# Kernel tuning notes

Hardware: AMD Instinct MI355X
Metric: run time of the kernel (lower is better)

## Reference

```python
import jax, jax.numpy as jnp
import numpy as np

NU, MI, D, H, DH, L, LAYERS = 80000, 40000, 64, 8, 8, 2, 3
EUI, EII, DT, DI, B = 1600000, 400000, 768, 512, 512


def setup_inputs() -> dict:
    rng = np.random.default_rng(0)
    u = rng.integers(0, NU, EUI); it = rng.integers(0, MI, EUI)
    du = np.maximum(np.bincount(u, minlength=NU), 1)
    di = np.maximum(np.bincount(it, minlength=MI), 1)
    val = (1.0 / np.sqrt(du[u] * di[it])).astype(np.float32)
    g_row = np.concatenate([u, it + NU]).astype(np.int32)
    g_col = np.concatenate([it + NU, u]).astype(np.int32)
    g_val = np.concatenate([val, val])

    def ig(seed):  # random item-item graph + self loops (dgl.add_self_loop)
        r = np.random.default_rng(seed)
        s = r.integers(0, MI, EII); d = r.integers(0, MI, EII); sl = np.arange(MI)
        return np.concatenate([s, sl]).astype(np.int32), np.concatenate([d, sl]).astype(np.int32)
    t_src, t_dst = ig(1); i_src, i_dst = ig(2)

    def xav(*shape):
        lim = np.sqrt(6.0 / (shape[-2] + shape[-1]))
        return rng.uniform(-lim, lim, shape).astype(np.float32)

    inp = dict(
        user_emb=(rng.standard_normal((NU, D)) * 0.1).astype(np.float32),
        item_emb=(rng.standard_normal((MI, D)) * 0.1).astype(np.float32),
        g_row=g_row, g_col=g_col, g_val=g_val,
        txt_feat=rng.standard_normal((MI, DT)).astype(np.float32),
        img_feat=rng.standard_normal((MI, DI)).astype(np.float32),
        t_src=t_src, t_dst=t_dst, i_src=i_src, i_dst=i_dst,
        txt_proj_w=xav(DT, D), txt_proj_b=np.zeros(D, np.float32),
        txt_fc_w=xav(L, D, D), txt_attn_l=xav(L, H, DH), txt_attn_r=xav(L, H, DH),
        txt_bias=np.zeros((L, D), np.float32),
        img_proj_w=xav(DI, D), img_proj_b=np.zeros(D, np.float32),
        img_fc_w=xav(L, D, D), img_attn_l=xav(L, H, DH), img_attn_r=xav(L, H, DH),
        img_bias=np.zeros((L, D), np.float32),
        delta_img=xav(D, D), delta_txt=xav(D, D),
        alpha=np.float32(0.05), beta=np.float32(0.8),
        ln_g=np.ones(D, np.float32), ln_b=np.zeros(D, np.float32),
        users=rng.integers(0, NU, B).astype(np.int32),
    )
    return {k: jnp.asarray(v) for k, v in inp.items()}


def _spmm(row, col, val, x, n):
    return jax.ops.segment_sum(val[:, None] * x[col], row, num_segments=n)


def _gat_layer(x, src, dst, fc_w, al, ar, b):
    N = x.shape[0]
    h = (x @ fc_w).reshape(N, H, DH)                 # [N,H,Dh]
    el = jnp.einsum('nhd,hd->nh', h, al)
    er = jnp.einsum('nhd,hd->nh', h, ar)
    e = jax.nn.leaky_relu(el[src] + er[dst], 0.2)    # [E,H]
    m = jax.ops.segment_max(e, dst, num_segments=N)
    a = jnp.exp(e - m[dst])
    a = a / jax.ops.segment_sum(a, dst, num_segments=N)[dst]
    out = jax.ops.segment_sum(a[:, :, None] * h[src], dst, num_segments=N)
    return (out + b.reshape(1, H, DH)).reshape(N, H * DH)


def _branch(feat, src, dst, pw, pb, fcw, al, ar, bias):
    x = feat @ pw + pb
    for l in range(L):
        x = jax.nn.leaky_relu(_gat_layer(x, src, dst, fcw[l], al[l], ar[l], bias[l]), 0.2)
    return x


def _sinkhorn(C, eps=0.01, iters=100):
    K = jnp.exp(-C / eps)
    d1, d2 = C.shape
    mu = jnp.full((d1,), 1.0 / d1, C.dtype)
    nu = jnp.full((d2,), 1.0 / d2, C.dtype)
    def body(_, uv):
        u, v = uv
        u = mu / (K @ v + 1e-8)
        v = nu / (K.T @ u + 1e-8)
        return (u, v)
    u, v = jax.lax.fori_loop(0, iters, body, (mu, nu))
    return u[:, None] * K * v[None, :]


def _ot_align(mm, st, delta):
    I = mm.shape[0]
    # mean_i (mm[i,k]-st[i,l])^2 * scale, without materializing [I,D,D]
    C = ((mm * mm).mean(0)[:, None] + (st * st).mean(0)[None, :] - 2.0 * (mm.T @ st) / I) * 100.0
    T = jax.lax.stop_gradient(_sinkhorn(C))  # torch computes T under no_grad
    return mm @ (T + delta)


def reference(user_emb, item_emb, g_row, g_col, g_val, txt_feat, img_feat,
              t_src, t_dst, i_src, i_dst,
              txt_proj_w, txt_proj_b, txt_fc_w, txt_attn_l, txt_attn_r, txt_bias,
              img_proj_w, img_proj_b, img_fc_w, img_attn_l, img_attn_r, img_bias,
              delta_img, delta_txt, alpha, beta, ln_g, ln_b, users):
    # LightGCN propagation
    cur = jnp.concatenate([user_emb, item_emb], 0)
    acc = cur
    for _ in range(LAYERS):
        cur = _spmm(g_row, g_col, g_val, cur, NU + MI)
        acc = acc + cur
    light = acc / (LAYERS + 1)
    zu, zi_cf = light[:NU], light[NU:]
    # multimodal GAT branches (dropout = eval mode)
    zi_txt = _branch(txt_feat, t_src, t_dst, txt_proj_w, txt_proj_b, txt_fc_w, txt_attn_l, txt_attn_r, txt_bias)
    zi_img = _branch(img_feat, i_src, i_dst, img_proj_w, img_proj_b, img_fc_w, img_attn_l, img_attn_r, img_bias)
    # OAT fusion
    a_img = _ot_align(zi_img, zi_cf, delta_img)
    a_txt = _ot_align(zi_txt, zi_cf, delta_txt)
    z = (1.0 - alpha - beta) * zi_cf + alpha * a_img + beta * a_txt
    mu = z.mean(-1, keepdims=True)
    var = ((z - mu) ** 2).mean(-1, keepdims=True)
    z = (z - mu) / jnp.sqrt(var + 1e-5) * ln_g + ln_b
    z = z / jnp.maximum(jnp.linalg.norm(z, axis=-1, keepdims=True), 1e-12)
    return zu[users] @ z.T  # [B, M_items] ratings
```

## Files before the change

### kernel.cpp

```cpp
#include <hip/hip_runtime.h>
#include <math.h>

__device__ __forceinline__ float lrelu(float x) { return x >= 0.f ? x : 0.2f * x; }

__global__ void hist_k(const int* __restrict__ row, int* __restrict__ tick, int E) {
  int e = blockIdx.x * 256 + threadIdx.x;
  if (e >= E) return;
  atomicAdd(&tick[row[e]], 1);
}

__global__ __launch_bounds__(256) void scan_part_k(const int* __restrict__ tick,
                                                   int* __restrict__ part, int N) {
  __shared__ int red[256];
  int base = blockIdx.x * 4096;
  int s = 0;
  for (int i = threadIdx.x; i < 4096; i += 256) {
    int idx = base + i;
    if (idx < N) s += tick[idx];
  }
  red[threadIdx.x] = s;
  __syncthreads();
  for (int off = 128; off > 0; off >>= 1) {
    if (threadIdx.x < off) red[threadIdx.x] += red[threadIdx.x + off];
    __syncthreads();
  }
  if (threadIdx.x == 0) part[blockIdx.x] = red[0];
}

__global__ __launch_bounds__(1024) void scan_partials_k(int* __restrict__ part, int nb) {
  __shared__ int sh[1024];
  int t = threadIdx.x;
  int v = (t < nb) ? part[t] : 0;
  sh[t] = v;
  __syncthreads();
  for (int off = 1; off < 1024; off <<= 1) {
    int x = sh[t];
    int y = (t >= off) ? sh[t - off] : 0;
    __syncthreads();
    sh[t] = x + y;
    __syncthreads();
  }
  if (t < nb) part[t] = (t == 0) ? 0 : sh[t - 1];
  if (t == 0) part[nb] = sh[nb - 1];
}

__global__ __launch_bounds__(256) void scan_apply_k(int* __restrict__ tick, int* __restrict__ rs,
                                                    const int* __restrict__ part, int N, int nb) {
  __shared__ int th[256];
  int base = blockIdx.x * 4096;
  int lo = base + threadIdx.x * 16;
  int vals[16];
  int s = 0;
#pragma unroll
  for (int j = 0; j < 16; ++j) {
    int idx = lo + j;
    int v = (idx < N) ? tick[idx] : 0;
    vals[j] = v;
    s += v;
  }
  th[threadIdx.x] = s;
  __syncthreads();
  for (int off = 1; off < 256; off <<= 1) {
    int x = th[threadIdx.x];
    int y = (threadIdx.x >= off) ? th[threadIdx.x - off] : 0;
    __syncthreads();
    th[threadIdx.x] = x + y;
    __syncthreads();
  }
  int excl = (threadIdx.x == 0) ? 0 : th[threadIdx.x - 1];
  int run = part[blockIdx.x] + excl;
#pragma unroll
  for (int j = 0; j < 16; ++j) {
    int idx = lo + j;
    if (idx < N) {
      rs[idx] = run;
      tick[idx] = run;
      run += vals[j];
    }
  }
  if (blockIdx.x == 0 && threadIdx.x == 0) rs[N] = part[nb];
}

__global__ void scatter_src_k(const int* __restrict__ src, const int* __restrict__ dst,
                              int* __restrict__ tick, int* __restrict__ srcs, int E) {
  int e = blockIdx.x * 256 + threadIdx.x;
  if (e >= E) return;
  int pos = atomicAdd(&tick[dst[e]], 1);
  srcs[pos] = src[e];
}

#define NBUCK_MAX 512

__global__ __launch_bounds__(256) void bin_count_k(const int* __restrict__ row,
                                                   int* __restrict__ bcnt, int E, int nbuck) {
  __shared__ int h[NBUCK_MAX];
  for (int i = threadIdx.x; i < nbuck; i += 256) h[i] = 0;
  __syncthreads();
  int base = blockIdx.x * 4096;
#pragma unroll
  for (int j = 0; j < 16; ++j) {
    int e = base + j * 256 + threadIdx.x;
    if (e < E) atomicAdd(&h[row[e] >> 8], 1);
  }
  __syncthreads();
  for (int i = threadIdx.x; i < nbuck; i += 256) {
    int c = h[i];
    if (c) atomicAdd(&bcnt[i], c);
  }
}

__global__ __launch_bounds__(512) void bucket_scan_k(int* __restrict__ base,
                                                     int* __restrict__ btick, int nbuck) {
  __shared__ int sh[512];
  int t = threadIdx.x;
  int v = (t < nbuck) ? base[t] : 0;
  sh[t] = v;
  __syncthreads();
  for (int off = 1; off < 512; off <<= 1) {
    int x = sh[t];
    int y = (t >= off) ? sh[t - off] : 0;
    __syncthreads();
    sh[t] = x + y;
    __syncthreads();
  }
  if (t < nbuck) {
    int excl = sh[t] - v;
    base[t] = excl;
    btick[t * 16] = excl;
    if (t == nbuck - 1) base[nbuck] = sh[t];
  }
}

__global__ __launch_bounds__(256) void bin_scatter_k(const int* __restrict__ row,
                                                     const int* __restrict__ col,
                                                     const float* __restrict__ val,
                                                     int* __restrict__ btick,
                                                     int* __restrict__ binned, int E, int nbuck) {
  __shared__ int cnt[NBUCK_MAX];
  __shared__ int bbase[NBUCK_MAX];
  for (int i = threadIdx.x; i < nbuck; i += 256) cnt[i] = 0;
  __syncthreads();
  int base = blockIdx.x * 4096;
  int erow[16], rk[16];
#pragma unroll
  for (int j = 0; j < 16; ++j) {
    int e = base + j * 256 + threadIdx.x;
    if (e < E) {
      int r = row[e];
      erow[j] = r;
      rk[j] = atomicAdd(&cnt[r >> 8], 1);
    } else {
      erow[j] = -1;
    }
  }
  __syncthreads();
  for (int i = threadIdx.x; i < nbuck; i += 256) {
    int c = cnt[i];
    bbase[i] = c ? atomicAdd(&btick[i * 16], c) : 0;
  }
  __syncthreads();
#pragma unroll
  for (int j = 0; j < 16; ++j) {
    int e = base + j * 256 + threadIdx.x;
    if (e < E) {
      int r = erow[j];
      int pos = bbase[r >> 8] + rk[j];
      int* p = binned + (size_t)pos * 3;
      p[0] = r;
      p[1] = col[e];
      p[2] = __float_as_int(val[e]);
    }
  }
}

__global__ __launch_bounds__(256) void csr_build_k(const int* __restrict__ bbase,
                                                   const int* __restrict__ binned,
                                                   int* __restrict__ rs,
                                                   int2* __restrict__ cv, int NT) {
  __shared__ int lh[256];
  __shared__ int tmp[256];
  int b = blockIdx.x;
  int t = threadIdx.x;
  int r0 = b << 8;
  int e0 = bbase[b], e1 = bbase[b + 1];
  lh[t] = 0;
  __syncthreads();
  for (int e = e0 + t; e < e1; e += 256) {
    int r = binned[(size_t)e * 3];
    atomicAdd(&lh[r - r0], 1);
  }
  __syncthreads();
  int c = lh[t];
  tmp[t] = c;
  __syncthreads();
  for (int off = 1; off < 256; off <<= 1) {
    int x = tmp[t];
    int y = (t >= off) ? tmp[t - off] : 0;
    __syncthreads();
    tmp[t] = x + y;
    __syncthreads();
  }
  int pos0 = e0 + tmp[t] - c;
  lh[t] = pos0;
  int r = r0 + t;
  if (r < NT) rs[r] = pos0;
  if (t == 0 && b == gridDim.x - 1) rs[NT] = e1;
  __syncthreads();
  for (int e = e0 + t; e < e1; e += 256) {
    const int* p = binned + (size_t)e * 3;
    int rr = p[0];
    int cc = p[1];
    int vv = p[2];
    int pos = atomicAdd(&lh[rr - r0], 1);
    cv[pos] = make_int2(cc, vv);
  }
}

template <int MODE>
__global__ __launch_bounds__(256) void spmm_csr(const int* __restrict__ rs,
                                                const int2* __restrict__ cv,
                                                const float* __restrict__ xs,
                                                const float* __restrict__ ue,
                                                const float* __restrict__ ie, int NUx,
                                                const float* __restrict__ l1,
                                                float* __restrict__ outp, int NT) {
  int wid = blockIdx.x * 4 + (threadIdx.x >> 6);
  int lane = threadIdx.x & 63;
  if (wid >= NT) return;
  int g = lane >> 4, sl = lane & 15;
  int e0 = rs[wid], e1 = rs[wid + 1];
  double ax = 0.0, ay = 0.0, az = 0.0, aw = 0.0;
  int e = e0;
#define GATHER_PTR(cx)                                                             \
  (MODE == 1 ? ((cx) < NUx ? (const float4*)ue + (size_t)(cx)*16                   \
                           : (const float4*)ie + (size_t)((cx)-NUx) * 16)          \
             : (const float4*)xs + (size_t)(cx)*16)
#define ACC4(vv, xx)                                                               \
  {                                                                                \
    double dv = (double)(vv);                                                      \
    ax += dv * (double)(xx).x;                                                     \
    ay += dv * (double)(xx).y;                                                     \
    az += dv * (double)(xx).z;                                                     \
    aw += dv * (double)(xx).w;                                                     \
  }
  for (; e + 16 <= e1; e += 16) {
    int2 c0 = cv[e + g];
    int2 c1 = cv[e + 4 + g];
    int2 c2 = cv[e + 8 + g];
    int2 c3 = cv[e + 12 + g];
    float4 x0 = GATHER_PTR(c0.x)[sl];
    float4 x1 = GATHER_PTR(c1.x)[sl];
    float4 x2 = GATHER_PTR(c2.x)[sl];
    float4 x3 = GATHER_PTR(c3.x)[sl];
    ACC4(__int_as_float(c0.y), x0);
    ACC4(__int_as_float(c1.y), x1);
    ACC4(__int_as_float(c2.y), x2);
    ACC4(__int_as_float(c3.y), x3);
  }
  for (; e + 4 <= e1; e += 4) {
    int2 c0 = cv[e + g];
    float4 x0 = GATHER_PTR(c0.x)[sl];
    ACC4(__int_as_float(c0.y), x0);
  }
  if (e < e1) {
    int idx = e + g;
    int2 c0 = make_int2(0, 0);
    if (idx < e1) c0 = cv[idx];
    float4 x0 = GATHER_PTR(c0.x)[sl];
    ACC4(__int_as_float(c0.y), x0);
  }
#undef ACC4
#undef GATHER_PTR
  ax += __shfl_xor(ax, 16, 64); ay += __shfl_xor(ay, 16, 64);
  az += __shfl_xor(az, 16, 64); aw += __shfl_xor(aw, 16, 64);
  ax += __shfl_xor(ax, 32, 64); ay += __shfl_xor(ay, 32, 64);
  az += __shfl_xor(az, 32, 64); aw += __shfl_xor(aw, 32, 64);
  if (g == 0) {
    size_t ro = (size_t)wid * 16 + sl;
    float4 s4 = make_float4((float)ax, (float)ay, (float)az, (float)aw);
    if (MODE == 2) {
      float4 x0 = (wid < NUx) ? ((const float4*)ue)[(size_t)wid * 16 + sl]
                              : ((const float4*)ie)[(size_t)(wid - NUx) * 16 + sl];
      float4 f1 = ((const float4*)l1)[ro];
      float4 f2 = ((const float4*)xs)[ro];
      float4 o;
      o.x = (x0.x + f1.x + f2.x + s4.x) * 0.25f;
      o.y = (x0.y + f1.y + f2.y + s4.y) * 0.25f;
      o.z = (x0.z + f1.z + f2.z + s4.z) * 0.25f;
      o.w = (x0.w + f1.w + f2.w + s4.w) * 0.25f;
      ((float4*)outp)[ro] = o;
    } else {
      ((float4*)outp)[ro] = s4;
    }
  }
}

template <int ACT>
__global__ __launch_bounds__(256) void gemm_n64(const float* __restrict__ A,
                                                const float* __restrict__ W,
                                                const float* __restrict__ bias,
                                                float* __restrict__ C, int M, int K) {
  __shared__ float AsT[32][68];
  __shared__ float Ws[32][64];
  int t = threadIdx.x;
  int row0 = blockIdx.x * 64;
  int tr = t >> 4, tc = t & 15;
  int lr = t >> 2, lq = (t & 3) * 8;
  int wk = t >> 3, wc = (t & 7) * 8;
  float acc[4][4] = {};
  for (int k0 = 0; k0 < K; k0 += 32) {
    float a8[8];
    if (row0 + lr < M) {
      const float* src = A + (size_t)(row0 + lr) * K + k0 + lq;
      float4 v0 = *(const float4*)(src);
      float4 v1 = *(const float4*)(src + 4);
      a8[0] = v0.x; a8[1] = v0.y; a8[2] = v0.z; a8[3] = v0.w;
      a8[4] = v1.x; a8[5] = v1.y; a8[6] = v1.z; a8[7] = v1.w;
    } else {
#pragma unroll
      for (int i = 0; i < 8; ++i) a8[i] = 0.f;
    }
    float4 w0 = *(const float4*)(W + (size_t)(k0 + wk) * 64 + wc);
    float4 w1 = *(const float4*)(W + (size_t)(k0 + wk) * 64 + wc + 4);
    __syncthreads();
#pragma unroll
    for (int i = 0; i < 8; ++i) AsT[lq + i][lr] = a8[i];
    *(float4*)&Ws[wk][wc] = w0;
    *(float4*)&Ws[wk][wc + 4] = w1;
    __syncthreads();
#pragma unroll
    for (int kki = 0; kki < 32; ++kki) {
      float4 av = *(const float4*)&AsT[kki][tr * 4];
      float4 wv = *(const float4*)&Ws[kki][tc * 4];
      acc[0][0] += av.x * wv.x; acc[0][1] += av.x * wv.y;
      acc[0][2] += av.x * wv.z; acc[0][3] += av.x * wv.w;
      acc[1][0] += av.y * wv.x; acc[1][1] += av.y * wv.y;
      acc[1][2] += av.y * wv.z; acc[1][3] += av.y * wv.w;
      acc[2][0] += av.z * wv.x; acc[2][1] += av.z * wv.y;
      acc[2][2] += av.z * wv.z; acc[2][3] += av.z * wv.w;
      acc[3][0] += av.w * wv.x; acc[3][1] += av.w * wv.y;
      acc[3][2] += av.w * wv.z; acc[3][3] += av.w * wv.w;
    }
  }
  float bv[4] = {0.f, 0.f, 0.f, 0.f};
  if (bias) *(float4*)bv = *(const float4*)(bias + tc * 4);
#pragma unroll
  for (int j = 0; j < 4; ++j) {
    int row = row0 + tr * 4 + j;
    if (row < M) {
      float o[4];
#pragma unroll
      for (int c = 0; c < 4; ++c) {
        float x = acc[j][c] + bv[c];
        o[c] = ACT ? lrelu(x) : x;
      }
      *(float4*)(C + (size_t)row * 64 + tc * 4) = *(float4*)o;
    }
  }
}

__global__ void attn_scores(const float* __restrict__ h, const float* __restrict__ al,
                            const float* __restrict__ ar, float* __restrict__ el,
                            float* __restrict__ er, int N) {
  long t = (long)blockIdx.x * blockDim.x + threadIdx.x;
  if (t >= (long)N * 8) return;
  int n = (int)(t >> 3), hh = (int)(t & 7);
  const float4* hp = (const float4*)(h + (size_t)n * 64 + hh * 8);
  float4 h0 = hp[0], h1 = hp[1];
  const float4* ap = (const float4*)(al + hh * 8);
  float4 a0 = ap[0], a1 = ap[1];
  const float4* bp = (const float4*)(ar + hh * 8);
  float4 b0 = bp[0], b1 = bp[1];
  float sl = h0.x * a0.x + h0.y * a0.y + h0.z * a0.z + h0.w * a0.w +
             h1.x * a1.x + h1.y * a1.y + h1.z * a1.z + h1.w * a1.w;
  float sr = h0.x * b0.x + h0.y * b0.y + h0.z * b0.z + h0.w * b0.w +
             h1.x * b1.x + h1.y * b1.y + h1.z * b1.z + h1.w * b1.w;
  el[t] = sl;
  er[t] = sr;
}

__global__ __launch_bounds__(256) void gat_agg(const int* __restrict__ rs,
                                               const int* __restrict__ srcs,
                                               const float* __restrict__ el,
                                               const float* __restrict__ er,
                                               const float* __restrict__ h,
                                               const float* __restrict__ bias,
                                               float* __restrict__ out, int N) {
  int d = blockIdx.x * 4 + (threadIdx.x >> 6);
  int lane = threadIdx.x & 63;
  if (d >= N) return;
  int hh = lane >> 3;
  int e0 = rs[d], e1 = rs[d + 1];
  float erd = er[(size_t)d * 8 + hh];
  float m = -INFINITY;
  int e = e0;
  for (; e + 8 <= e1; e += 8) {
    int s8[8];
#pragma unroll
    for (int j = 0; j < 8; ++j) s8[j] = srcs[e + j];
    float v8[8];
#pragma unroll
    for (int j = 0; j < 8; ++j) v8[j] = el[(size_t)s8[j] * 8 + hh];
#pragma unroll
    for (int j = 0; j < 8; ++j) m = fmaxf(m, lrelu(v8[j] + erd));
  }
  for (; e < e1; ++e) {
    int s = srcs[e];
    float v = lrelu(el[(size_t)s * 8 + hh] + erd);
    m = fmaxf(m, v);
  }
  double den = 0.0, acc = 0.0;
  e = e0;
  for (; e + 4 <= e1; e += 4) {
    int s4[4];
#pragma unroll
    for (int j = 0; j < 4; ++j) s4[j] = srcs[e + j];
    float v4[4];
#pragma unroll
    for (int j = 0; j < 4; ++j) v4[j] = el[(size_t)s4[j] * 8 + hh];
    float h4[4];
#pragma unroll
    for (int j = 0; j < 4; ++j) h4[j] = h[(size_t)s4[j] * 64 + lane];
#pragma unroll
    for (int j = 0; j < 4; ++j) {
      float a = expf(lrelu(v4[j] + erd) - m);
      den += (double)a;
      acc += (double)a * (double)h4[j];
    }
  }
  for (; e < e1; ++e) {
    int s = srcs[e];
    float v = lrelu(el[(size_t)s * 8 + hh] + erd);
    float a = expf(v - m);
    den += (double)a;
    acc += (double)a * (double)h[(size_t)s * 64 + lane];
  }
  out[(size_t)d * 64 + lane] = lrelu((float)(acc / den) + bias[lane]);
}

__global__ __launch_bounds__(256) void gram_part_k(const float* __restrict__ mm0,
                                                   const float* __restrict__ mm1,
                                                   const float* __restrict__ st,
                                                   float* __restrict__ part, int N) {
  __shared__ float ms[128][64];
  __shared__ float ss[128][64];
  const float* mm = blockIdx.y ? mm1 : mm0;
  float* po = part + ((size_t)blockIdx.y * gridDim.x + blockIdx.x) * 4224;
  int t = threadIdx.x;
  int n0 = blockIdx.x * 128;
  for (int idx = t; idx < 128 * 16; idx += 256) {
    int r = idx >> 4, q = (idx & 15) * 4;
    float4 a, b;
    if (n0 + r < N) {
      a = *(const float4*)(mm + (size_t)(n0 + r) * 64 + q);
      b = *(const float4*)(st + (size_t)(n0 + r) * 64 + q);
    } else {
      a = make_float4(0, 0, 0, 0);
      b = make_float4(0, 0, 0, 0);
    }
    *(float4*)&ms[r][q] = a;
    *(float4*)&ss[r][q] = b;
  }
  __syncthreads();
  if (t < 64) {
    float s = 0.f;
    for (int n = 0; n < 128; ++n) { float x = ms[n][t]; s += x * x; }
    po[4096 + t] = s;
  } else if (t < 128) {
    int c = t - 64;
    float s = 0.f;
    for (int n = 0; n < 128; ++n) { float x = ss[n][c]; s += x * x; }
    po[4160 + c] = s;
  }
  int i = t >> 2, jb = (t & 3) * 16;
  float acc[16] = {};
  for (int n = 0; n < 128; ++n) {
    float a = ms[n][i];
#pragma unroll
    for (int j = 0; j < 16; ++j) acc[j] += a * ss[n][jb + j];
  }
#pragma unroll
  for (int j = 0; j < 16; j += 4)
    *(float4*)&po[i * 64 + jb + j] = *(float4*)&acc[j];
}

__global__ __launch_bounds__(256) void gram_reduce_k(const float* __restrict__ part,
                                                     double* __restrict__ G_all, int nb) {
  int idx = blockIdx.x * 256 + threadIdx.x;
  if (idx >= 4224) return;
  int br = blockIdx.y;
  const float* p = part + (size_t)br * nb * 4224 + idx;
  double s = 0.0;
  int b = 0;
  for (; b + 4 <= nb; b += 4) {
    s += ((double)p[(size_t)b * 4224] + (double)p[(size_t)(b + 1) * 4224]) +
         ((double)p[(size_t)(b + 2) * 4224] + (double)p[(size_t)(b + 3) * 4224]);
  }
  for (; b < nb; ++b) s += (double)p[(size_t)b * 4224];
  G_all[(size_t)br * 4224 + idx] = s;
}

__global__ __launch_bounds__(256) void sinkhorn2_k(const double* __restrict__ G_all,
                                                   const float* __restrict__ delta_txt,
                                                   const float* __restrict__ delta_img,
                                                   float* __restrict__ TD_all, int N) {
  __shared__ double u_s[64], v_s[64];
  int b = blockIdx.x;
  const double* G = G_all + (size_t)b * 4224;
  const double* mmsq = G + 4096;
  const double* stsq = G + 4160;
  const float* delta = b ? delta_img : delta_txt;
  float* TD = TD_all + (size_t)b * 4096;
  int t = threadIdx.x;
  int r = t >> 2, p = t & 3;
  int j0 = p * 16;
  double invN = 1.0 / (double)N;
  double Kr[16], Kc[16];
  double rq = mmsq[r] * invN;
  double cq = stsq[r] * invN;
#pragma unroll
  for (int q = 0; q < 16; ++q) {
    int j = j0 + q;
    double Crj = (rq + stsq[j] * invN - 2.0 * G[r * 64 + j] * invN) * 100.0;
    Kr[q] = exp(-Crj / 0.01);
    double Cjr = (mmsq[j] * invN + cq - 2.0 * G[j * 64 + r] * invN) * 100.0;
    Kc[q] = exp(-Cjr / 0.01);
  }
  if (p == 0) {
    u_s[r] = 1.0 / 64.0;
    v_s[r] = 1.0 / 64.0;
  }
  __syncthreads();
  for (int it = 0; it < 100; ++it) {
    double s0 = 0.0, s1 = 0.0, s2 = 0.0, s3 = 0.0;
#pragma unroll
    for (int q = 0; q < 16; q += 4) {
      s0 += Kr[q] * v_s[j0 + q];
      s1 += Kr[q + 1] * v_s[j0 + q + 1];
      s2 += Kr[q + 2] * v_s[j0 + q + 2];
      s3 += Kr[q + 3] * v_s[j0 + q + 3];
    }
    double s = (s0 + s1) + (s2 + s3);
    s += __shfl_xor(s, 1, 64);
    s += __shfl_xor(s, 2, 64);
    if (p == 0) u_s[r] = (1.0 / 64.0) / (s + 1e-8);
    __syncthreads();
    double z0 = 0.0, z1 = 0.0, z2 = 0.0, z3 = 0.0;
#pragma unroll
    for (int q = 0; q < 16; q += 4) {
      z0 += Kc[q] * u_s[j0 + q];
      z1 += Kc[q + 1] * u_s[j0 + q + 1];
      z2 += Kc[q + 2] * u_s[j0 + q + 2];
      z3 += Kc[q + 3] * u_s[j0 + q + 3];
    }
    double z = (z0 + z1) + (z2 + z3);
    z += __shfl_xor(z, 1, 64);
    z += __shfl_xor(z, 2, 64);
    if (p == 0) v_s[r] = (1.0 / 64.0) / (z + 1e-8);
    __syncthreads();
  }
  double ur = u_s[r];
#pragma unroll
  for (int q = 0; q < 16; ++q) {
    int j = j0 + q;
    TD[r * 64 + j] = (float)(ur * Kr[q] * v_s[j]) + delta[r * 64 + j];
  }
}

__global__ __launch_bounds__(256) void fuse_ln(const float* __restrict__ zi_cf,
                                               const float* __restrict__ a_img,
                                               const float* __restrict__ a_txt,
                                               const float* __restrict__ g,
                                               const float* __restrict__ b,
                                               const float* __restrict__ alpha_p,
                                               const float* __restrict__ beta_p,
                                               float* __restrict__ z, int N) {
  long gt = (long)blockIdx.x * blockDim.x + threadIdx.x;
  long row = gt >> 6;
  int lane = (int)(gt & 63);
  if (row >= N) return;
  float al = *alpha_p, be = *beta_p;
  size_t idx = (size_t)row * 64 + lane;
  float v = (1.f - al - be) * zi_cf[idx] + al * a_img[idx] + be * a_txt[idx];
  float s = v;
  for (int o = 32; o; o >>= 1) s += __shfl_xor(s, o, 64);
  float mean = s * (1.f / 64.f);
  float dv = v - mean;
  float q = dv * dv;
  for (int o = 32; o; o >>= 1) q += __shfl_xor(q, o, 64);
  float var = q * (1.f / 64.f);
  float zn = dv / sqrtf(var + 1e-5f) * g[lane] + b[lane];
  float n2 = zn * zn;
  for (int o = 32; o; o >>= 1) n2 += __shfl_xor(n2, o, 64);
  float nrm = fmaxf(sqrtf(n2), 1e-12f);
  z[idx] = zn / nrm;
}

__global__ void gather_users(const float* __restrict__ acc, const int* __restrict__ users,
                             float* __restrict__ zu, int B) {
  int t = blockIdx.x * 256 + threadIdx.x;
  if (t >= B * 64) return;
  int b = t >> 6, d = t & 63;
  zu[t] = acc[(size_t)users[b] * 64 + d];
}

__global__ __launch_bounds__(256) void final_gemm(const float* __restrict__ zu,
                                                  const float* __restrict__ z,
                                                  float* __restrict__ out, int B, int NI) {
  __shared__ float zu_s[64][65];
  __shared__ float zs_s[64][65];
  int t = threadIdx.x;
  int i0 = blockIdx.x * 64;
  int b0 = blockIdx.y * 64;
  {
    int r = t >> 2, q = (t & 3) * 16;
    float vals[16];
    if (b0 + r < B) {
      const float* src = zu + (size_t)(b0 + r) * 64 + q;
#pragma unroll
      for (int j = 0; j < 16; j += 4) {
        float4 v = *(const float4*)(src + j);
        vals[j] = v.x; vals[j + 1] = v.y; vals[j + 2] = v.z; vals[j + 3] = v.w;
      }
    } else {
#pragma unroll
      for (int j = 0; j < 16; ++j) vals[j] = 0.f;
    }
#pragma unroll
    for (int j = 0; j < 16; ++j) zu_s[r][q + j] = vals[j];
    const float* zsrc = z + (size_t)(i0 + r) * 64 + q;
#pragma unroll
    for (int j = 0; j < 16; j += 4) {
      float4 v = *(const float4*)(zsrc + j);
      zs_s[r][q + j] = v.x; zs_s[r][q + j + 1] = v.y;
      zs_s[r][q + j + 2] = v.z; zs_s[r][q + j + 3] = v.w;
    }
  }
  __syncthreads();
  int tu = t >> 4, tc = t & 15;
  float acc[4][4] = {};
  for (int d = 0; d < 64; ++d) {
    float au[4], zv[4];
#pragma unroll
    for (int j = 0; j < 4; ++j) au[j] = zu_s[tu * 4 + j][d];
#pragma unroll
    for (int j = 0; j < 4; ++j) zv[j] = zs_s[tc * 4 + j][d];
#pragma unroll
    for (int j = 0; j < 4; ++j)
#pragma unroll
      for (int k = 0; k < 4; ++k) acc[j][k] += au[j] * zv[k];
  }
#pragma unroll
  for (int j = 0; j < 4; ++j) {
    int bb = b0 + tu * 4 + j;
    if (bb < B) {
      float4 o = make_float4(acc[j][0], acc[j][1], acc[j][2], acc[j][3]);
      *(float4*)(out + (size_t)bb * NI + i0 + tc * 4) = o;
    }
  }
}

static inline int cdiv_i(long a, long b) { return (int)((a + b - 1) / b); }

extern "C" void kernel_launch(void* const* d_in, const int* in_sizes, int n_in,
                              void* d_out, int out_size, void* d_ws, size_t ws_size,
                              hipStream_t stream) {
  const float* user_emb = (const float*)d_in[0];
  const float* item_emb = (const float*)d_in[1];
  const int* g_row = (const int*)d_in[2];
  const int* g_col = (const int*)d_in[3];
  const float* g_val = (const float*)d_in[4];
  const float* txt_feat = (const float*)d_in[5];
  const float* img_feat = (const float*)d_in[6];
  const int* t_src = (const int*)d_in[7];
  const int* t_dst = (const int*)d_in[8];
  const int* i_src = (const int*)d_in[9];
  const int* i_dst = (const int*)d_in[10];
  const float* txt_proj_w = (const float*)d_in[11];
  const float* txt_proj_b = (const float*)d_in[12];
  const float* txt_fc_w = (const float*)d_in[13];
  const float* txt_attn_l = (const float*)d_in[14];
  const float* txt_attn_r = (const float*)d_in[15];
  const float* txt_bias = (const float*)d_in[16];
  const float* img_proj_w = (const float*)d_in[17];
  const float* img_proj_b = (const float*)d_in[18];
  const float* img_fc_w = (const float*)d_in[19];
  const float* img_attn_l = (const float*)d_in[20];
  const float* img_attn_r = (const float*)d_in[21];
  const float* img_bias = (const float*)d_in[22];
  const float* delta_img = (const float*)d_in[23];
  const float* delta_txt = (const float*)d_in[24];
  const float* alpha = (const float*)d_in[25];
  const float* beta = (const float*)d_in[26];
  const float* ln_g = (const float*)d_in[27];
  const float* ln_b = (const float*)d_in[28];
  const int* users = (const int*)d_in[29];

  const int NU = in_sizes[0] / 64;
  const int MI = in_sizes[1] / 64;
  const int EG = in_sizes[2];
  const int DT = in_sizes[5] / MI;
  const int DI = in_sizes[6] / MI;
  const int ET = in_sizes[7];
  const int B = in_sizes[29];
  const int NT = NU + MI;
  const size_t NT64 = (size_t)NT * 64;
  const size_t MI64 = (size_t)MI * 64;
  const size_t MI8 = (size_t)MI * 8;

  float* cur = (float*)d_ws;
  float* nxt = cur + NT64;
  int* rs = (int*)(nxt + NT64);
  int* tick = rs + (NT + 1);
  int2* cv = (int2*)(tick + (NT + 1));
  int* rs_g = (int*)(cv + EG);
  int* tick_g = rs_g + (MI + 1);
  int* gat_src = tick_g + (MI + 1);
  int* part = gat_src + ET;
  float* TD_all = (float*)(part + 1025);
  uintptr_t gaddr = ((uintptr_t)(TD_all + 8192) + 15) & ~(uintptr_t)15;
  double* G_all = (double*)gaddr;
  float* zu_sel = (float*)(G_all + 2 * 4224);

  float* acc = (float*)d_out;

  float* xb = cur;
  float* hb = cur + MI64;
  float* el = cur + 2 * MI64;
  float* er = el + MI8;
  float* zi_txt = nxt + MI64;
  float* zi_img = nxt + 2 * MI64;
  float* a_txt = cur;
  float* a_img = cur + MI64;
  float* zbuf = nxt;

  const int nbuck = (NT + 255) >> 8;
  int* binned = (int*)cur;
  int* btick = binned + (((size_t)3 * EG + 15) & ~(size_t)15);
  int* bbase = part;
  hipMemsetAsync(bbase, 0, (nbuck + 1) * sizeof(int), stream);
  bin_count_k<<<cdiv_i(EG, 4096), 256, 0, stream>>>(g_row, bbase, EG, nbuck);
  bucket_scan_k<<<1, 512, 0, stream>>>(bbase, btick, nbuck);
  bin_scatter_k<<<cdiv_i(EG, 4096), 256, 0, stream>>>(g_row, g_col, g_val, btick, binned, EG,
                                                      nbuck);
  csr_build_k<<<nbuck, 256, 0, stream>>>(bbase, binned, rs, cv, NT);

  const int spmmGrid = cdiv_i(NT, 4);
  spmm_csr<1><<<spmmGrid, 256, 0, stream>>>(rs, cv, nullptr, user_emb, item_emb, NU,
                                            nullptr, cur, NT);
  spmm_csr<0><<<spmmGrid, 256, 0, stream>>>(rs, cv, cur, nullptr, nullptr, 0,
                                            nullptr, nxt, NT);
  spmm_csr<2><<<spmmGrid, 256, 0, stream>>>(rs, cv, nxt, user_emb, item_emb, NU,
                                            cur, acc, NT);
  const float* zi_cf = acc + (size_t)NU * 64;

  const float* feats[2] = {txt_feat, img_feat};
  const int dfeat[2] = {DT, DI};
  const float* pw[2] = {txt_proj_w, img_proj_w};
  const float* pb[2] = {txt_proj_b, img_proj_b};
  const float* fcw[2] = {txt_fc_w, img_fc_w};
  const float* alw[2] = {txt_attn_l, img_attn_l};
  const float* arw[2] = {txt_attn_r, img_attn_r};
  const float* bsw[2] = {txt_bias, img_bias};
  const int* esrc[2] = {t_src, i_src};
  const int* edst[2] = {t_dst, i_dst};
  float* zi[2] = {zi_txt, zi_img};

  const int gemmGrid = cdiv_i(MI, 64);
  const int aggGrid = cdiv_i(MI, 4);
  const int nbg = cdiv_i(MI, 4096);
  for (int br = 0; br < 2; ++br) {
    hipMemsetAsync(tick_g, 0, (MI + 1) * sizeof(int), stream);
    hist_k<<<cdiv_i(ET, 256), 256, 0, stream>>>(edst[br], tick_g, ET);
    scan_part_k<<<nbg, 256, 0, stream>>>(tick_g, part, MI);
    scan_partials_k<<<1, 1024, 0, stream>>>(part, nbg);
    scan_apply_k<<<nbg, 256, 0, stream>>>(tick_g, rs_g, part, MI, nbg);
    scatter_src_k<<<cdiv_i(ET, 256), 256, 0, stream>>>(esrc[br], edst[br], tick_g, gat_src, ET);

    gemm_n64<0><<<gemmGrid, 256, 0, stream>>>(feats[br], pw[br], pb[br], xb, MI, dfeat[br]);
    for (int l = 0; l < 2; ++l) {
      gemm_n64<0><<<gemmGrid, 256, 0, stream>>>(xb, fcw[br] + l * 4096, nullptr, hb, MI, 64);
      attn_scores<<<cdiv_i((long)MI * 8, 256), 256, 0, stream>>>(hb, alw[br] + l * 64,
                                                                 arw[br] + l * 64, el, er, MI);
      gat_agg<<<aggGrid, 256, 0, stream>>>(rs_g, gat_src, el, er, hb, bsw[br] + l * 64,
                                           (l == 1) ? zi[br] : xb, MI);
    }
  }

  const int ngb = cdiv_i(MI, 128);
  float* gpart = cur;
  {
    dim3 gg(ngb, 2);
    gram_part_k<<<gg, 256, 0, stream>>>(zi_txt, zi_img, zi_cf, gpart, MI);
    dim3 rg(cdiv_i(4224, 256), 2);
    gram_reduce_k<<<rg, 256, 0, stream>>>(gpart, G_all, ngb);
  }
  sinkhorn2_k<<<2, 256, 0, stream>>>(G_all, delta_txt, delta_img, TD_all, MI);
  gemm_n64<0><<<gemmGrid, 256, 0, stream>>>(zi_txt, TD_all, nullptr, a_txt, MI, 64);
  gemm_n64<0><<<gemmGrid, 256, 0, stream>>>(zi_img, TD_all + 4096, nullptr, a_img, MI, 64);

  fuse_ln<<<cdiv_i((long)MI * 64, 256), 256, 0, stream>>>(zi_cf, a_img, a_txt, ln_g, ln_b, alpha,
                                                          beta, zbuf, MI);

  gather_users<<<cdiv_i((long)B * 64, 256), 256, 0, stream>>>(acc, users, zu_sel, B);

  dim3 fg(MI / 64, cdiv_i(B, 64));
  final_gemm<<<fg, 256, 0, stream>>>(zu_sel, zbuf, (float*)d_out, B, MI);
}
```

Baseline: 1.133 ms.

## Batch text and image GAT branches into paired launches and single-pass softmax

```diff
diff --git a/kernel.cpp b/kernel.cpp
--- a/kernel.cpp
+++ b/kernel.cpp
@@ -3,14 +3,22 @@
 
 __device__ __forceinline__ float lrelu(float x) { return x >= 0.f ? x : 0.2f * x; }
 
-__global__ void hist_k(const int* __restrict__ row, int* __restrict__ tick, int E) {
+__global__ void hist2_k(const int* __restrict__ d0, const int* __restrict__ d1,
+                        int* __restrict__ t0, int* __restrict__ t1, int E) {
   int e = blockIdx.x * 256 + threadIdx.x;
   if (e >= E) return;
-  atomicAdd(&tick[row[e]], 1);
-}
-
-__global__ __launch_bounds__(256) void scan_part_k(const int* __restrict__ tick,
-                                                   int* __restrict__ part, int N) {
+  if (blockIdx.y == 0)
+    atomicAdd(&t0[d0[e]], 1);
+  else
+    atomicAdd(&t1[d1[e]], 1);
+}
+
+__global__ __launch_bounds__(256) void scan_part2_k(const int* __restrict__ t0,
+                                                    const int* __restrict__ t1,
+                                                    int* __restrict__ p0,
+                                                    int* __restrict__ p1, int N) {
+  const int* tick = blockIdx.y ? t1 : t0;
+  int* part = blockIdx.y ? p1 : p0;
   __shared__ int red[256];
   int base = blockIdx.x * 4096;
   int s = 0;
@@ -27,7 +35,9 @@
   if (threadIdx.x == 0) part[blockIdx.x] = red[0];
 }
 
-__global__ __launch_bounds__(1024) void scan_partials_k(int* __restrict__ part, int nb) {
+__global__ __launch_bounds__(1024) void scan_partials2_k(int* __restrict__ p0,
+                                                         int* __restrict__ p1, int nb) {
+  int* part = blockIdx.y ? p1 : p0;
   __shared__ int sh[1024];
   int t = threadIdx.x;
   int v = (t < nb) ? part[t] : 0;
@@ -44,8 +54,13 @@
   if (t == 0) part[nb] = sh[nb - 1];
 }
 
-__global__ __launch_bounds__(256) void scan_apply_k(int* __restrict__ tick, int* __restrict__ rs,
-                                                    const int* __restrict__ part, int N, int nb) {
+__global__ __launch_bounds__(256) void scan_apply2_k(int* __restrict__ t0, int* __restrict__ t1,
+                                                     int* __restrict__ r0, int* __restrict__ r1,
+                                                     const int* __restrict__ p0,
+                                                     const int* __restrict__ p1, int N, int nb) {
+  int* tick = blockIdx.y ? t1 : t0;
+  int* rs = blockIdx.y ? r1 : r0;
+  const int* part = blockIdx.y ? p1 : p0;
   __shared__ int th[256];
   int base = blockIdx.x * 4096;
   int lo = base + threadIdx.x * 16;
@@ -81,12 +96,19 @@
   if (blockIdx.x == 0 && threadIdx.x == 0) rs[N] = part[nb];
 }
 
-__global__ void scatter_src_k(const int* __restrict__ src, const int* __restrict__ dst,
-                              int* __restrict__ tick, int* __restrict__ srcs, int E) {
+__global__ void scatter_src2_k(const int* __restrict__ s0, const int* __restrict__ d0,
+                               const int* __restrict__ s1, const int* __restrict__ d1,
+                               int* __restrict__ t0, int* __restrict__ t1,
+                               int* __restrict__ o0, int* __restrict__ o1, int E) {
   int e = blockIdx.x * 256 + threadIdx.x;
   if (e >= E) return;
-  int pos = atomicAdd(&tick[dst[e]], 1);
-  srcs[pos] = src[e];
+  if (blockIdx.y == 0) {
+    int pos = atomicAdd(&t0[d0[e]], 1);
+    o0[pos] = s0[e];
+  } else {
+    int pos = atomicAdd(&t1[d1[e]], 1);
+    o1[pos] = s1[e];
+  }
 }
 
 #define NBUCK_MAX 512
@@ -296,10 +318,19 @@
 }
 
 template <int ACT>
-__global__ __launch_bounds__(256) void gemm_n64(const float* __restrict__ A,
-                                                const float* __restrict__ W,
-                                                const float* __restrict__ bias,
-                                                float* __restrict__ C, int M, int K) {
+__global__ __launch_bounds__(256) void gemm2_n64(const float* __restrict__ A0,
+                                                 const float* __restrict__ A1,
+                                                 const float* __restrict__ W0,
+                                                 const float* __restrict__ W1,
+                                                 const float* __restrict__ b0,
+                                                 const float* __restrict__ b1,
+                                                 float* __restrict__ C0,
+                                                 float* __restrict__ C1, int M, int K0, int K1) {
+  const float* A = blockIdx.y ? A1 : A0;
+  const float* W = blockIdx.y ? W1 : W0;
+  const float* bias = blockIdx.y ? b1 : b0;
+  float* C = blockIdx.y ? C1 : C0;
+  const int K = blockIdx.y ? K1 : K0;
   __shared__ float AsT[32][68];
   __shared__ float Ws[32][64];
   int t = threadIdx.x;
@@ -359,40 +390,62 @@
   }
 }
 
-__global__ void attn_scores(const float* __restrict__ h, const float* __restrict__ al,
-                            const float* __restrict__ ar, float* __restrict__ el,
-                            float* __restrict__ er, int N) {
+__global__ void attn2_scores(const float* __restrict__ h0, const float* __restrict__ h1,
+                             const float* __restrict__ al0, const float* __restrict__ al1,
+                             const float* __restrict__ ar0, const float* __restrict__ ar1,
+                             float* __restrict__ el0, float* __restrict__ el1,
+                             float* __restrict__ er0, float* __restrict__ er1, int N) {
   long t = (long)blockIdx.x * blockDim.x + threadIdx.x;
   if (t >= (long)N * 8) return;
+  const float* h = blockIdx.y ? h1 : h0;
+  const float* al = blockIdx.y ? al1 : al0;
+  const float* ar = blockIdx.y ? ar1 : ar0;
+  float* el = blockIdx.y ? el1 : el0;
+  float* er = blockIdx.y ? er1 : er0;
   int n = (int)(t >> 3), hh = (int)(t & 7);
   const float4* hp = (const float4*)(h + (size_t)n * 64 + hh * 8);
-  float4 h0 = hp[0], h1 = hp[1];
+  float4 hv0 = hp[0], hv1 = hp[1];
   const float4* ap = (const float4*)(al + hh * 8);
   float4 a0 = ap[0], a1 = ap[1];
   const float4* bp = (const float4*)(ar + hh * 8);
   float4 b0 = bp[0], b1 = bp[1];
-  float sl = h0.x * a0.x + h0.y * a0.y + h0.z * a0.z + h0.w * a0.w +
-             h1.x * a1.x + h1.y * a1.y + h1.z * a1.z + h1.w * a1.w;
-  float sr = h0.x * b0.x + h0.y * b0.y + h0.z * b0.z + h0.w * b0.w +
-             h1.x * b1.x + h1.y * b1.y + h1.z * b1.z + h1.w * b1.w;
+  float sl = hv0.x * a0.x + hv0.y * a0.y + hv0.z * a0.z + hv0.w * a0.w +
+             hv1.x * a1.x + hv1.y * a1.y + hv1.z * a1.z + hv1.w * a1.w;
+  float sr = hv0.x * b0.x + hv0.y * b0.y + hv0.z * b0.z + hv0.w * b0.w +
+             hv1.x * b1.x + hv1.y * b1.y + hv1.z * b1.z + hv1.w * b1.w;
   el[t] = sl;
   er[t] = sr;
 }
 
-__global__ __launch_bounds__(256) void gat_agg(const int* __restrict__ rs,
-                                               const int* __restrict__ srcs,
-                                               const float* __restrict__ el,
-                                               const float* __restrict__ er,
-                                               const float* __restrict__ h,
-                                               const float* __restrict__ bias,
-                                               float* __restrict__ out, int N) {
+__global__ __launch_bounds__(256) void gat_agg2(const int* __restrict__ rsa,
+                                                const int* __restrict__ rsb,
+                                                const int* __restrict__ sa,
+                                                const int* __restrict__ sb,
+                                                const float* __restrict__ ela,
+                                                const float* __restrict__ elb,
+                                                const float* __restrict__ era,
+                                                const float* __restrict__ erb,
+                                                const float* __restrict__ ha,
+                                                const float* __restrict__ hbp,
+                                                const float* __restrict__ ba,
+                                                const float* __restrict__ bb,
+                                                float* __restrict__ oa,
+                                                float* __restrict__ ob, int N) {
+  int br = blockIdx.y;
+  const int* rs = br ? rsb : rsa;
+  const int* srcs = br ? sb : sa;
+  const float* el = br ? elb : ela;
+  const float* er = br ? erb : era;
+  const float* h = br ? hbp : ha;
+  const float* bias = br ? bb : ba;
+  float* out = br ? ob : oa;
   int d = blockIdx.x * 4 + (threadIdx.x >> 6);
   int lane = threadIdx.x & 63;
   if (d >= N) return;
   int hh = lane >> 3;
   int e0 = rs[d], e1 = rs[d + 1];
   float erd = er[(size_t)d * 8 + hh];
-  float m = -INFINITY;
+  double den = 0.0, acc = 0.0;
   int e = e0;
   for (; e + 8 <= e1; e += 8) {
     int s8[8];
@@ -401,37 +454,19 @@
     float v8[8];
 #pragma unroll
     for (int j = 0; j < 8; ++j) v8[j] = el[(size_t)s8[j] * 8 + hh];
-#pragma unroll
-    for (int j = 0; j < 8; ++j) m = fmaxf(m, lrelu(v8[j] + erd));
+    float h8[8];
+#pragma unroll
+    for (int j = 0; j < 8; ++j) h8[j] = h[(size_t)s8[j] * 64 + lane];
+#pragma unroll
+    for (int j = 0; j < 8; ++j) {
+      float a = expf(lrelu(v8[j] + erd));
+      den += (double)a;
+      acc += (double)a * (double)h8[j];
+    }
   }
   for (; e < e1; ++e) {
     int s = srcs[e];
-    float v = lrelu(el[(size_t)s * 8 + hh] + erd);
-    m = fmaxf(m, v);
-  }
-  double den = 0.0, acc = 0.0;
-  e = e0;
-  for (; e + 4 <= e1; e += 4) {
-    int s4[4];
-#pragma unroll
-    for (int j = 0; j < 4; ++j) s4[j] = srcs[e + j];
-    float v4[4];
-#pragma unroll
-    for (int j = 0; j < 4; ++j) v4[j] = el[(size_t)s4[j] * 8 + hh];
-    float h4[4];
-#pragma unroll
-    for (int j = 0; j < 4; ++j) h4[j] = h[(size_t)s4[j] * 64 + lane];
-#pragma unroll
-    for (int j = 0; j < 4; ++j) {
-      float a = expf(lrelu(v4[j] + erd) - m);
-      den += (double)a;
-      acc += (double)a * (double)h4[j];
-    }
-  }
-  for (; e < e1; ++e) {
-    int s = srcs[e];
-    float v = lrelu(el[(size_t)s * 8 + hh] + erd);
-    float a = expf(v - m);
+    float a = expf(lrelu(el[(size_t)s * 8 + hh] + erd));
     den += (double)a;
     acc += (double)a * (double)h[(size_t)s * 64 + lane];
   }
@@ -723,6 +758,16 @@
   float* zu_sel = (float*)(G_all + 2 * 4224);
 
   float* acc = (float*)d_out;
+  float* base2 = (float*)d_out + NT64;
+  float* xb2 = base2;
+  float* hb2 = base2 + MI64;
+  float* el2 = base2 + 2 * MI64;
+  float* er2 = el2 + MI8;
+  int* ints2 = (int*)(er2 + MI8);
+  int* rs_g2 = ints2;
+  int* tick_g2 = rs_g2 + (MI + 1);
+  int* gat_src2 = tick_g2 + (MI + 1);
+  int* part2 = gat_src2 + ET;
 
   float* xb = cur;
   float* hb = cur + MI64;
@@ -754,36 +799,37 @@
                                             cur, acc, NT);
   const float* zi_cf = acc + (size_t)NU * 64;
 
-  const float* feats[2] = {txt_feat, img_feat};
-  const int dfeat[2] = {DT, DI};
-  const float* pw[2] = {txt_proj_w, img_proj_w};
-  const float* pb[2] = {txt_proj_b, img_proj_b};
-  const float* fcw[2] = {txt_fc_w, img_fc_w};
-  const float* alw[2] = {txt_attn_l, img_attn_l};
-  const float* arw[2] = {txt_attn_r, img_attn_r};
-  const float* bsw[2] = {txt_bias, img_bias};
-  const int* esrc[2] = {t_src, i_src};
-  const int* edst[2] = {t_dst, i_dst};
-  float* zi[2] = {zi_txt, zi_img};
-
   const int gemmGrid = cdiv_i(MI, 64);
   const int aggGrid = cdiv_i(MI, 4);
   const int nbg = cdiv_i(MI, 4096);
-  for (int br = 0; br < 2; ++br) {
-    hipMemsetAsync(tick_g, 0, (MI + 1) * sizeof(int), stream);
-    hist_k<<<cdiv_i(ET, 256), 256, 0, stream>>>(edst[br], tick_g, ET);
-    scan_part_k<<<nbg, 256, 0, stream>>>(tick_g, part, MI);
-    scan_partials_k<<<1, 1024, 0, stream>>>(part, nbg);
-    scan_apply_k<<<nbg, 256, 0, stream>>>(tick_g, rs_g, part, MI, nbg);
-    scatter_src_k<<<cdiv_i(ET, 256), 256, 0, stream>>>(esrc[br], edst[br], tick_g, gat_src, ET);
-
-    gemm_n64<0><<<gemmGrid, 256, 0, stream>>>(feats[br], pw[br], pb[br], xb, MI, dfeat[br]);
+
+  hipMemsetAsync(tick_g, 0, (MI + 1) * sizeof(int), stream);
+  hipMemsetAsync(tick_g2, 0, (MI + 1) * sizeof(int), stream);
+  {
+    dim3 eh(cdiv_i(ET, 256), 2);
+    dim3 sp(nbg, 2);
+    hist2_k<<<eh, 256, 0, stream>>>(t_dst, i_dst, tick_g, tick_g2, ET);
+    scan_part2_k<<<sp, 256, 0, stream>>>(tick_g, tick_g2, part, part2, MI);
+    scan_partials2_k<<<dim3(1, 2), 1024, 0, stream>>>(part, part2, nbg);
+    scan_apply2_k<<<sp, 256, 0, stream>>>(tick_g, tick_g2, rs_g, rs_g2, part, part2, MI, nbg);
+    scatter_src2_k<<<eh, 256, 0, stream>>>(t_src, t_dst, i_src, i_dst, tick_g, tick_g2,
+                                           gat_src, gat_src2, ET);
+  }
+  {
+    dim3 gg(gemmGrid, 2);
+    dim3 ag(aggGrid, 2);
+    dim3 at(cdiv_i((long)MI * 8, 256), 2);
+    gemm2_n64<0><<<gg, 256, 0, stream>>>(txt_feat, img_feat, txt_proj_w, img_proj_w,
+                                         txt_proj_b, img_proj_b, xb, xb2, MI, DT, DI);
     for (int l = 0; l < 2; ++l) {
-      gemm_n64<0><<<gemmGrid, 256, 0, stream>>>(xb, fcw[br] + l * 4096, nullptr, hb, MI, 64);
-      attn_scores<<<cdiv_i((long)MI * 8, 256), 256, 0, stream>>>(hb, alw[br] + l * 64,
-                                                                 arw[br] + l * 64, el, er, MI);
-      gat_agg<<<aggGrid, 256, 0, stream>>>(rs_g, gat_src, el, er, hb, bsw[br] + l * 64,
-                                           (l == 1) ? zi[br] : xb, MI);
+      gemm2_n64<0><<<gg, 256, 0, stream>>>(xb, xb2, txt_fc_w + l * 4096, img_fc_w + l * 4096,
+                                           nullptr, nullptr, hb, hb2, MI, 64, 64);
+      attn2_scores<<<at, 256, 0, stream>>>(hb, hb2, txt_attn_l + l * 64, img_attn_l + l * 64,
+                                           txt_attn_r + l * 64, img_attn_r + l * 64,
+                                           el, el2, er, er2, MI);
+      gat_agg2<<<ag, 256, 0, stream>>>(rs_g, rs_g2, gat_src, gat_src2, el, el2, er, er2,
+                                       hb, hb2, txt_bias + l * 64, img_bias + l * 64,
+                                       (l == 1) ? zi_txt : xb, (l == 1) ? zi_img : xb2, MI);
     }
   }
 
@@ -796,8 +842,11 @@
     gram_reduce_k<<<rg, 256, 0, stream>>>(gpart, G_all, ngb);
   }
   sinkhorn2_k<<<2, 256, 0, stream>>>(G_all, delta_txt, delta_img, TD_all, MI);
-  gemm_n64<0><<<gemmGrid, 256, 0, stream>>>(zi_txt, TD_all, nullptr, a_txt, MI, 64);
-  gemm_n64<0><<<gemmGrid, 256, 0, stream>>>(zi_img, TD_all + 4096, nullptr, a_img, MI, 64);
+  {
+    dim3 gg(gemmGrid, 2);
+    gemm2_n64<0><<<gg, 256, 0, stream>>>(zi_txt, zi_img, TD_all, TD_all + 4096, nullptr, nullptr,
+                                         a_txt, a_img, MI, 64, 64);
+  }
 
   fuse_ln<<<cdiv_i((long)MI * 64, 256), 256, 0, stream>>>(zi_cf, a_img, a_txt, ln_g, ln_b, alpha,
                                                           beta, zbuf, MI);
```

Measured after the change: 1.042 ms. 1.09x faster.
